# Kernel optimization log

Measured on AMD Instinct MI355X. Metric: run time of the kernel, lower is better.

The kernel has to match this reference:

```python
import jax, jax.numpy as jnp
import numpy as np

FILTERS = [1, 3, 7, 9]
BN_EPS = 1e-5


def _conv1d(x, w, b):
    # x: [B, C, L], w: [O, I, F] (torch Conv1d layout), 'same' padding for odd F
    pad = (w.shape[-1] - 1) // 2
    y = jax.lax.conv_general_dilated(
        x, w, window_strides=(1,), padding=[(pad, pad)],
        dimension_numbers=("NCH", "OIH", "NCH"))
    return y + b[None, :, None]


def _bn_elu(x, gamma, beta):
    # BatchNorm1d in training mode: biased batch stats over (batch, length)
    m = jnp.mean(x, axis=(0, 2), keepdims=True)
    v = jnp.var(x, axis=(0, 2), keepdims=True)
    xn = (x - m) * jax.lax.rsqrt(v + BN_EPS)
    return jax.nn.elu(xn * gamma[None, :, None] + beta[None, :, None])


def setup_inputs() -> dict:
    key = jax.random.key(0)
    ks = jax.random.split(key, 32)
    b, h, l, lk, dk = 8, 8, 1024, 1024, 64
    inp = {
        "Q": jax.random.normal(ks[0], (b, h, l, dk), jnp.float32),
        "K": jax.random.normal(ks[1], (b, h, lk, dk), jnp.float32),
        "V": jax.random.normal(ks[2], (b, h, lk, dk), jnp.float32),
        "W_pq": jax.random.normal(ks[3], (1, dk), jnp.float32) * 0.1,
        "W_bq": jax.random.normal(ks[4], (dk, 1), jnp.float32) * 0.1,
        "W_bk": jax.random.normal(ks[5], (dk, 1), jnp.float32) * 0.1,
        "bn_g": jax.random.uniform(ks[6], (h,), jnp.float32, 0.5, 1.5),
        "bn_b": jax.random.normal(ks[7], (h,), jnp.float32) * 0.1,
        "attn_mask": jnp.ones((1,), dtype=bool),
    }
    for i, f in enumerate(FILTERS):
        s = 1.0 / np.sqrt(h * f)
        inp[f"cq_w{i}"] = jax.random.normal(ks[8 + i], (h, h, f), jnp.float32) * s
        inp[f"cq_b{i}"] = jax.random.normal(ks[12 + i], (h,), jnp.float32) * 0.05
        inp[f"ck_w{i}"] = jax.random.normal(ks[16 + i], (h, h, f), jnp.float32) * s
        inp[f"ck_b{i}"] = jax.random.normal(ks[20 + i], (h,), jnp.float32) * 0.05
    return inp


def reference(Q, K, V, W_pq, W_bq, W_bk,
              cq_w0, cq_b0, cq_w1, cq_b1, cq_w2, cq_b2, cq_w3, cq_b3,
              ck_w0, ck_b0, ck_w1, ck_b1, ck_w2, ck_b2, ck_w3, ck_b3,
              bn_g, bn_b, attn_mask):
    b, h, l, dk = Q.shape
    lk = K.shape[2]
    nf = len(FILTERS)
    # proj_q applied to BOTH Q and K (proj_k is dead in the original code)
    q = jnp.einsum("bhld,d->bhl", Q, W_pq[0])  # [b,h,l]
    k = jnp.einsum("bhld,d->bhl", K, W_pq[0])  # [b,h,lk]
    cq = [(cq_w0, cq_b0), (cq_w1, cq_b1), (cq_w2, cq_b2), (cq_w3, cq_b3)]
    ck = [(ck_w0, ck_b0), (ck_w1, ck_b1), (ck_w2, ck_b2), (ck_w3, ck_b3)]
    Q_l = [_bn_elu(_conv1d(q, w, bb), bn_g, bn_b) for w, bb in cq]
    K_l = [_bn_elu(_conv1d(k, w, bb), bn_g, bn_b) for w, bb in ck]
    # replicate torch.cat(dim=0) + reshape(b,h,nf*len) flat-order semantics
    Q_p = jnp.concatenate(Q_l, axis=0).reshape(b, h, nf * l)    # [b,h,4l]
    K_p = jnp.concatenate(K_l, axis=0).reshape(b, h, nf * lk)   # [b,h,4lk]
    Qt = jax.lax.top_k(Q_p, l)[0]                               # [b,h,l]
    Km = jnp.mean(K_p.reshape(b, h, nf, lk), axis=2)            # [b,h,lk]
    Kt = jax.lax.top_k(Km, lk)[0]                               # descending sort
    Qb = Qt[..., None] * W_bq[:, 0]                             # [b,h,l,dk]
    Kb = Kt[..., None] * W_bk[:, 0]                             # [b,h,lk,dk]
    scores = jnp.einsum("bhqd,bhkd->bhqk", Qb, Kb) / np.float32(np.sqrt(dk))
    attn = jax.nn.softmax(scores, axis=-1)
    context = jnp.einsum("bhqk,bhkd->bhqd", attn, V)
    return context, attn
```

## Files before the change

### kernel.cpp

```cpp
#include <hip/hip_runtime.h>
#include <hip/hip_bf16.h>
#include <math.h>

namespace {
constexpr int CONV_OFF = 131072;
constexpr int PS_OFF   = 655360;
constexpr int PSS_OFF  = 659456;
constexpr int QT_OFF   = 663552;
constexpr int KT_OFF   = 729088;

typedef short bf16x8 __attribute__((ext_vector_type(8)));
typedef float f32x4 __attribute__((ext_vector_type(4)));

union BF8 {
  bf16x8 v;
  short s[8];
};

__device__ inline float bn_elu(float v, float mean, float rstd, float g,
                               float be) {
  const float x = (v - mean) * rstd * g + be;
  return x > 0.f ? x : expm1f(x);
}

__device__ inline void cswap(float& a, float& b, bool up) {
  const float mx = fmaxf(a, b), mn = fminf(a, b);
  a = up ? mx : mn;
  b = up ? mn : mx;
}

__device__ inline void wsort1024(float v[16], int lane) {
#pragma unroll
  for (int k = 2; k <= 1024; k <<= 1) {
#pragma unroll
    for (int j = 512; j >= 16; j >>= 1) {
      if (j <= (k >> 1)) {
        const int lj = j >> 4;
        const bool up = ((lane & (k >> 4)) == 0);
        const bool keep = (up == ((lane & lj) == 0));
#pragma unroll
        for (int e = 0; e < 16; ++e) {
          const float p = __shfl_xor(v[e], lj, 64);
          v[e] = keep ? fmaxf(v[e], p) : fminf(v[e], p);
        }
      }
    }
#pragma unroll
    for (int j = 8; j >= 1; j >>= 1) {
      if (j <= (k >> 1)) {
#pragma unroll
        for (int e = 0; e < 16; ++e) {
          if ((e & j) == 0) {
            bool up;
            if (k >= 32)
              up = ((lane & (k >> 4)) == 0);
            else if (k == 16)
              up = ((lane & 1) == 0);
            else
              up = ((e & k) == 0);
            cswap(v[e], v[e ^ j], up);
          }
        }
      }
    }
  }
}

__device__ inline void wmerge1024(float v[16], int lane) {
#pragma unroll
  for (int lj = 32; lj >= 1; lj >>= 1) {
    const bool keep = ((lane & lj) == 0);
#pragma unroll
    for (int e = 0; e < 16; ++e) {
      const float p = __shfl_xor(v[e], lj, 64);
      v[e] = keep ? fmaxf(v[e], p) : fminf(v[e], p);
    }
  }
#pragma unroll
  for (int j = 8; j >= 1; j >>= 1)
#pragma unroll
    for (int e = 0; e < 16; ++e)
      if ((e & j) == 0) cswap(v[e], v[e ^ j], true);
}

template <int F>
__device__ inline void pc_filter(const float* __restrict__ xs,
                                 const float* __restrict__ wsm, float bias,
                                 float* __restrict__ outp, int grp, int ln,
                                 int lq, float& sv, float& qv) {
  constexpr int pad = (F - 1) / 2;
  sv = 0.f;
  qv = 0.f;
#pragma unroll
  for (int i = 0; i < 4; ++i) {
    const int l = ln + 32 * i;
    float acc = bias;
#pragma unroll
    for (int c = 0; c < 8; ++c) {
      const float* xrow = &xs[c * 136 + l + 4 - pad];
      const float* wrow = &wsm[(grp * 8 + c) * F];
#pragma unroll
      for (int f = 0; f < F; ++f) acc = fmaf(xrow[f], wrow[f], acc);
    }
    outp[grp * 1024 + lq * 128 + l] = acc;
    sv += acc;
    qv = fmaf(acc, acc, qv);
  }
}

__global__ __launch_bounds__(256) void projconv_kernel(
    const float* __restrict__ Q, const float* __restrict__ K,
    const float* __restrict__ Wpq,
    const float* __restrict__ wq0, const float* __restrict__ bq0,
    const float* __restrict__ wq1, const float* __restrict__ bq1,
    const float* __restrict__ wq2, const float* __restrict__ bq2,
    const float* __restrict__ wq3, const float* __restrict__ bq3,
    const float* __restrict__ wk0, const float* __restrict__ bk0,
    const float* __restrict__ wk1, const float* __restrict__ bk1,
    const float* __restrict__ wk2, const float* __restrict__ bk2,
    const float* __restrict__ wk3, const float* __restrict__ bk3,
    float* __restrict__ conv, float* __restrict__ psum,
    float* __restrict__ psumsq) {
  __shared__ float xs[8 * 136];
  __shared__ float wsh[64];
  __shared__ float wsm[1280];
  __shared__ float bsm[32];
  const int tid = threadIdx.x;
  const int blk = blockIdx.x;
  const int path = blk >> 6, bb = (blk >> 3) & 7, lq = blk & 7;
  const float* X = path == 0 ? Q : K;
  const float* w0 = path == 0 ? wq0 : wk0;
  const float* w1 = path == 0 ? wq1 : wk1;
  const float* w2 = path == 0 ? wq2 : wk2;
  const float* w3 = path == 0 ? wq3 : wk3;
  const float* b0 = path == 0 ? bq0 : bk0;
  const float* b1 = path == 0 ? bq1 : bk1;
  const float* b2 = path == 0 ? bq2 : bk2;
  const float* b3 = path == 0 ? bq3 : bk3;
  if (tid < 64) wsh[tid] = Wpq[tid];
  for (int e = tid; e < 64; e += 256) wsm[e] = w0[e];
  for (int e = tid; e < 192; e += 256) wsm[64 + e] = w1[e];
  for (int e = tid; e < 448; e += 256) wsm[256 + e] = w2[e];
  for (int e = tid; e < 576; e += 256) wsm[704 + e] = w3[e];
  if (tid < 8)
    bsm[tid] = b0[tid];
  else if (tid < 16)
    bsm[tid] = b1[tid - 8];
  else if (tid < 24)
    bsm[tid] = b2[tid - 16];
  else if (tid < 32)
    bsm[tid] = b3[tid - 24];
  __syncthreads();
  for (int w = tid; w < 1088; w += 256) {
    const int c = w / 136, p = w - c * 136;
    const int gl = lq * 128 + p - 4;
    float acc = 0.f;
    if (gl >= 0 && gl < 1024) {
      const float* src = X + ((size_t)(bb * 8 + c) * 1024 + gl) * 64;
#pragma unroll
      for (int j = 0; j < 16; ++j) {
        const float4 x4 = *(const float4*)(src + j * 4);
        acc = fmaf(x4.x, wsh[j * 4 + 0], acc);
        acc = fmaf(x4.y, wsh[j * 4 + 1], acc);
        acc = fmaf(x4.z, wsh[j * 4 + 2], acc);
        acc = fmaf(x4.w, wsh[j * 4 + 3], acc);
      }
    }
    xs[c * 136 + p] = acc;
  }
  __syncthreads();
  const int grp = tid >> 5, ln = tid & 31;
  float sv, qv;
#define PC_DO(fi, F, WOFF)                                                   \
  pc_filter<F>(xs, wsm + WOFF, bsm[fi * 8 + grp],                            \
               conv + (size_t)((path * 4 + fi) * 8 + bb) * 8192, grp, ln,    \
               lq, sv, qv);                                                  \
  _Pragma("unroll") for (int m = 16; m >= 1; m >>= 1) {                      \
    sv += __shfl_xor(sv, m, 64);                                             \
    qv += __shfl_xor(qv, m, 64);                                             \
  }                                                                          \
  if (ln == 0) {                                                             \
    psum[((path * 4 + fi) * 8 + grp) * 64 + bb * 8 + lq] = sv;               \
    psumsq[((path * 4 + fi) * 8 + grp) * 64 + bb * 8 + lq] = qv;             \
  }
  PC_DO(0, 1, 0)
  PC_DO(1, 3, 64)
  PC_DO(2, 7, 256)
  PC_DO(3, 9, 704)
#undef PC_DO
}

__global__ __launch_bounds__(256) void sortmerge2_kernel(
    const float* __restrict__ conv, const float* __restrict__ psum,
    const float* __restrict__ psumsq, const float* __restrict__ bng,
    const float* __restrict__ bnb, float* __restrict__ Qt,
    float* __restrict__ Kt) {
  __shared__ float s1[1024];
  __shared__ float s2[1024];
  const int tid = threadIdx.x, blk = blockIdx.x;
  const int wv = tid >> 6, l = tid & 63;
  float v[16];
  if (blk < 64) {
    const int row = blk;
    const int hp = row & 7, fi = row >> 4;
    const int bb = ((row >> 3) & 1) * 4 + (hp >> 1);
    const int hh = (hp & 1) * 4 + wv;
    const int ch = fi * 8 + hh;
    float sval = 0.f;
    if (l < 2) {
      const float* src = (l == 0) ? psum : psumsq;
#pragma unroll
      for (int i = 0; i < 64; ++i) sval += src[ch * 64 + i];
    }
    const float mean = __shfl(sval, 0, 64) * (1.f / 8192.f);
    const float msq = __shfl(sval, 1, 64) * (1.f / 8192.f);
    const float rstd = rsqrtf(fmaxf(msq - mean * mean, 0.f) + 1e-5f);
    const float g = bng[hh], be = bnb[hh];
    const float* base = conv + (size_t)(fi * 8 + bb) * 8192 + hh * 1024;
#pragma unroll
    for (int j = 0; j < 4; ++j) {
      const float4 x = *(const float4*)&base[l * 16 + j * 4];
      v[j * 4 + 0] = bn_elu(x.x, mean, rstd, g, be);
      v[j * 4 + 1] = bn_elu(x.y, mean, rstd, g, be);
      v[j * 4 + 2] = bn_elu(x.z, mean, rstd, g, be);
      v[j * 4 + 3] = bn_elu(x.w, mean, rstd, g, be);
    }
    wsort1024(v, l);
    if (wv == 1)
#pragma unroll
      for (int e = 0; e < 16; ++e) s1[l * 16 + e] = v[e];
    if (wv == 3)
#pragma unroll
      for (int e = 0; e < 16; ++e) s2[l * 16 + e] = v[e];
    __syncthreads();
    if (wv == 0) {
#pragma unroll
      for (int e = 0; e < 16; ++e) v[e] = fmaxf(v[e], s1[1023 - (l * 16 + e)]);
      wmerge1024(v, l);
    } else if (wv == 2) {
#pragma unroll
      for (int e = 0; e < 16; ++e) v[e] = fmaxf(v[e], s2[1023 - (l * 16 + e)]);
      wmerge1024(v, l);
#pragma unroll
      for (int e = 0; e < 16; ++e) s2[l * 16 + e] = v[e];
    }
    __syncthreads();
    if (wv == 0) {
#pragma unroll
      for (int e = 0; e < 16; ++e) v[e] = fmaxf(v[e], s2[1023 - (l * 16 + e)]);
      wmerge1024(v, l);
      float* qd = Qt + (size_t)row * 1024 + l * 16;
#pragma unroll
      for (int j = 0; j < 4; ++j)
        *(float4*)&qd[j * 4] =
            make_float4(v[j * 4], v[j * 4 + 1], v[j * 4 + 2], v[j * 4 + 3]);
    }
  } else {
    const int row = (blk - 64) * 4 + wv;
    const int hp = row & 7, fi = row >> 4;
    const int bb = ((row >> 3) & 1) * 4 + (hp >> 1);
    const int chk = 32 + fi * 8 + (hp & 1) * 4;
    float sval = 0.f;
    if (l < 8) {
      const float* src = (l < 4) ? psum : psumsq;
      const int ch = chk + (l & 3);
#pragma unroll
      for (int i = 0; i < 64; ++i) sval += src[ch * 64 + i];
    }
    float cm[4], cr[4];
#pragma unroll
    for (int j = 0; j < 4; ++j) {
      const float mean = __shfl(sval, j, 64) * (1.f / 8192.f);
      const float msq = __shfl(sval, j + 4, 64) * (1.f / 8192.f);
      cm[j] = mean;
      cr[j] = rsqrtf(fmaxf(msq - mean * mean, 0.f) + 1e-5f);
    }
#pragma unroll
    for (int e = 0; e < 16; ++e) v[e] = 0.f;
#pragma unroll
    for (int j = 0; j < 4; ++j) {
      const int hh = (hp & 1) * 4 + j;
      const float g = bng[hh], be = bnb[hh];
      const float* base =
          conv + (size_t)(4 + fi) * 64 * 1024 + (size_t)bb * 8192 + hh * 1024;
#pragma unroll
      for (int jj = 0; jj < 4; ++jj) {
        const float4 x = *(const float4*)&base[l * 16 + jj * 4];
        v[jj * 4 + 0] += bn_elu(x.x, cm[j], cr[j], g, be);
        v[jj * 4 + 1] += bn_elu(x.y, cm[j], cr[j], g, be);
        v[jj * 4 + 2] += bn_elu(x.z, cm[j], cr[j], g, be);
        v[jj * 4 + 3] += bn_elu(x.w, cm[j], cr[j], g, be);
      }
    }
#pragma unroll
    for (int e = 0; e < 16; ++e) v[e] *= 0.25f;
    wsort1024(v, l);
    float* kd = Kt + (size_t)row * 1024 + l * 16;
#pragma unroll
    for (int j = 0; j < 4; ++j)
      *(float4*)&kd[j * 4] =
          make_float4(v[j * 4], v[j * 4 + 1], v[j * 4 + 2], v[j * 4 + 3]);
  }
}

__global__ __launch_bounds__(256, 4) void attn5_kernel(
    const float* __restrict__ V, const float* __restrict__ Qt,
    const float* __restrict__ Kt, const float* __restrict__ Wbq,
    const float* __restrict__ Wbk, float* __restrict__ ctx,
    float* __restrict__ attn) {
  __shared__ float Kts[1024];
  __shared__ float sq[64], mq[64], rz[64];
  __shared__ short Vhi[2][8 * 64 * 8];
  __shared__ short Vlo[2][8 * 64 * 8];
  const int tid = threadIdx.x;
  const int b = blockIdx.x;
  const int bh = ((b & 7) << 3) | ((b >> 3) & 7);
  const int qt = b >> 6;
  const int qbase = qt * 64;
  const int lane0 = tid & 63;
  float cval;
  {
    float d = Wbq[lane0] * Wbk[lane0];
#pragma unroll
    for (int mm = 32; mm >= 1; mm >>= 1) d += __shfl_xor(d, mm, 64);
    cval = d * 0.125f;
  }
  const float* Ktg = Kt + (size_t)bh * 1024;
  for (int t = tid; t < 1024; t += 256) Kts[t] = Ktg[t];
  const float kHi = Ktg[0], kLo = Ktg[1023];
  if (tid < 64) {
    const float s = cval * Qt[(size_t)bh * 1024 + qbase + tid];
    sq[tid] = s;
    mq[tid] = fmaxf(s * kHi, s * kLo);
  }
  __syncthreads();
  {
    const int row = tid >> 2, qtr = tid & 3;
    const float s = sq[row], m = mq[row];
    float z = 0.f;
    const int k0 = qtr * 256;
    for (int k = 0; k < 256; ++k) z += __expf(fmaf(s, Kts[k0 + k], -m));
    z += __shfl_xor(z, 1, 64);
    z += __shfl_xor(z, 2, 64);
    if (qtr == 0) rz[row] = 1.f / z;
  }
  __syncthreads();

  const int wv = tid >> 6, l = tid & 63;
  const int l15 = l & 15, l4 = l >> 4;
  const int q = wv * 16 + l15;
  const float s = sq[q], m = mq[q], r = rz[q];
  f32x4 acc[4];
#pragma unroll
  for (int dt = 0; dt < 4; ++dt) acc[dt] = (f32x4){0.f, 0.f, 0.f, 0.f};

  const float* Vb = V + (size_t)bh * 65536;
  float* arow = attn + ((size_t)bh << 20) + (size_t)qbase * 1024;
  const int dV = tid & 63, kqV = tid >> 6;

  for (int ch = 0; ch < 16; ++ch) {
    const int kc = ch * 64;
    const int buf = ch & 1;
    float vreg[2][8];
#pragma unroll
    for (int g = 0; g < 2; ++g) {
      const int ko = kqV + g * 4;
      const float* vs = Vb + (size_t)(kc + ko * 8) * 64 + dV;
#pragma unroll
      for (int i = 0; i < 8; ++i) vreg[g][i] = vs[i * 64];
    }
    bf16x8 ahi[2], alo[2];
#pragma unroll
    for (int ks = 0; ks < 2; ++ks) {
      const int kb = kc + ks * 32 + l4 * 8;
      const float4 kv0 = *(const float4*)&Kts[kb];
      const float4 kv1 = *(const float4*)&Kts[kb + 4];
      float e[8];
      e[0] = __expf(fmaf(s, kv0.x, -m)) * r;
      e[1] = __expf(fmaf(s, kv0.y, -m)) * r;
      e[2] = __expf(fmaf(s, kv0.z, -m)) * r;
      e[3] = __expf(fmaf(s, kv0.w, -m)) * r;
      e[4] = __expf(fmaf(s, kv1.x, -m)) * r;
      e[5] = __expf(fmaf(s, kv1.y, -m)) * r;
      e[6] = __expf(fmaf(s, kv1.z, -m)) * r;
      e[7] = __expf(fmaf(s, kv1.w, -m)) * r;
      float* ag = arow + (size_t)q * 1024 + kb;
      *(float4*)ag = make_float4(e[0], e[1], e[2], e[3]);
      *(float4*)(ag + 4) = make_float4(e[4], e[5], e[6], e[7]);
      BF8 H, L;
#pragma unroll
      for (int i = 0; i < 8; ++i) {
        const __hip_bfloat16 hb = __float2bfloat16(e[i]);
        H.s[i] = __bfloat16_as_short(hb);
        L.s[i] =
            __bfloat16_as_short(__float2bfloat16(e[i] - __bfloat162float(hb)));
      }
      ahi[ks] = H.v;
      alo[ks] = L.v;
    }
#pragma unroll
    for (int g = 0; g < 2; ++g) {
      const int ko = kqV + g * 4;
      BF8 H, L;
#pragma unroll
      for (int i = 0; i < 8; ++i) {
        const float f = vreg[g][i];
        const __hip_bfloat16 hb = __float2bfloat16(f);
        H.s[i] = __bfloat16_as_short(hb);
        L.s[i] =
            __bfloat16_as_short(__float2bfloat16(f - __bfloat162float(hb)));
      }
      *(bf16x8*)&Vhi[buf][(ko * 64 + dV) * 8] = H.v;
      *(bf16x8*)&Vlo[buf][(ko * 64 + dV) * 8] = L.v;
    }
    __syncthreads();
#pragma unroll
    for (int ks = 0; ks < 2; ++ks) {
      const int ko = ks * 4 + l4;
#pragma unroll
      for (int dt = 0; dt < 4; ++dt) {
        const bf16x8 bhv =
            *(const bf16x8*)&Vhi[buf][(ko * 64 + dt * 16 + l15) * 8];
        const bf16x8 blv =
            *(const bf16x8*)&Vlo[buf][(ko * 64 + dt * 16 + l15) * 8];
        acc[dt] = __builtin_amdgcn_mfma_f32_16x16x32_bf16(ahi[ks], bhv,
                                                          acc[dt], 0, 0, 0);
        acc[dt] = __builtin_amdgcn_mfma_f32_16x16x32_bf16(ahi[ks], blv,
                                                          acc[dt], 0, 0, 0);
        acc[dt] = __builtin_amdgcn_mfma_f32_16x16x32_bf16(alo[ks], bhv,
                                                          acc[dt], 0, 0, 0);
      }
    }
  }
  float* cb = ctx + ((size_t)bh * 1024 + qbase + wv * 16 + l4 * 4) * 64 + l15;
#pragma unroll
  for (int dt = 0; dt < 4; ++dt)
#pragma unroll
    for (int rr = 0; rr < 4; ++rr) cb[(size_t)rr * 64 + dt * 16] = acc[dt][rr];
}

}

extern "C" void kernel_launch(void* const* d_in, const int* in_sizes, int n_in,
                              void* d_out, int out_size, void* d_ws,
                              size_t ws_size, hipStream_t stream) {
  const float* Q = (const float*)d_in[0];
  const float* K = (const float*)d_in[1];
  const float* V = (const float*)d_in[2];
  const float* Wpq = (const float*)d_in[3];
  const float* Wbq = (const float*)d_in[4];
  const float* Wbk = (const float*)d_in[5];
  const float* bng = (const float*)d_in[6];
  const float* bnb = (const float*)d_in[7];
  const float* cqw[4] = {(const float*)d_in[9], (const float*)d_in[13],
                         (const float*)d_in[17], (const float*)d_in[21]};
  const float* cqb[4] = {(const float*)d_in[10], (const float*)d_in[14],
                         (const float*)d_in[18], (const float*)d_in[22]};
  const float* ckw[4] = {(const float*)d_in[11], (const float*)d_in[15],
                         (const float*)d_in[19], (const float*)d_in[23]};
  const float* ckb[4] = {(const float*)d_in[12], (const float*)d_in[16],
                         (const float*)d_in[20], (const float*)d_in[24]};

  float* ws = (float*)d_ws;
  float* conv = ws + CONV_OFF;
  float* psum = ws + PS_OFF;
  float* psumsq = ws + PSS_OFF;
  float* Qtp = ws + QT_OFF;
  float* Ktp = ws + KT_OFF;
  float* ctx = (float*)d_out;
  float* attn = ctx + (size_t)8 * 8 * 1024 * 64;

  projconv_kernel<<<128, 256, 0, stream>>>(
      Q, K, Wpq, cqw[0], cqb[0], cqw[1], cqb[1], cqw[2], cqb[2], cqw[3],
      cqb[3], ckw[0], ckb[0], ckw[1], ckb[1], ckw[2], ckb[2], ckw[3], ckb[3],
      conv, psum, psumsq);
  sortmerge2_kernel<<<80, 256, 0, stream>>>(conv, psum, psumsq, bng, bnb, Qtp,
                                            Ktp);
  attn5_kernel<<<1024, 256, 0, stream>>>(V, Qtp, Ktp, Wbq, Wbk, ctx, attn);
}
```

Measured before the change: 116.8 us.

## Split projection-conv into finer tiles and spread K-path averaging across waves

Halves the sequence tile per projconv block (64 instead of 128 positions), doubling the grid to 256 blocks, and doubles the partial-sum slots to match. In the sort kernel, the K path now gives each row its own block, with four waves each doing the BN+ELU for one channel in parallel and combining through shared memory before one wave sorts. It also compacts the workspace offsets. The aim is more parallelism in the two pre-attention stages, at the cost of more halo recomputation, more partial sums to reduce, and an extra barrier.

New measurement: 110.2 us. 1.06x faster.

```diff
diff --git a/kernel.cpp b/kernel.cpp
--- a/kernel.cpp
+++ b/kernel.cpp
@@ -3,11 +3,11 @@
 #include <math.h>
 
 namespace {
-constexpr int CONV_OFF = 131072;
-constexpr int PS_OFF   = 655360;
-constexpr int PSS_OFF  = 659456;
-constexpr int QT_OFF   = 663552;
-constexpr int KT_OFF   = 729088;
+constexpr int CONV_OFF = 0;
+constexpr int PS_OFF   = 524288;
+constexpr int PSS_OFF  = 532480;
+constexpr int QT_OFF   = 540672;
+constexpr int KT_OFF   = 606208;
 
 typedef short bf16x8 __attribute__((ext_vector_type(8)));
 typedef float f32x4 __attribute__((ext_vector_type(4)));
@@ -92,17 +92,17 @@
   sv = 0.f;
   qv = 0.f;
 #pragma unroll
-  for (int i = 0; i < 4; ++i) {
+  for (int i = 0; i < 2; ++i) {
     const int l = ln + 32 * i;
     float acc = bias;
 #pragma unroll
     for (int c = 0; c < 8; ++c) {
-      const float* xrow = &xs[c * 136 + l + 4 - pad];
+      const float* xrow = &xs[c * 72 + l + 4 - pad];
       const float* wrow = &wsm[(grp * 8 + c) * F];
 #pragma unroll
       for (int f = 0; f < F; ++f) acc = fmaf(xrow[f], wrow[f], acc);
     }
-    outp[grp * 1024 + lq * 128 + l] = acc;
+    outp[grp * 1024 + lq * 64 + l] = acc;
     sv += acc;
     qv = fmaf(acc, acc, qv);
   }
@@ -121,13 +121,13 @@
     const float* __restrict__ wk3, const float* __restrict__ bk3,
     float* __restrict__ conv, float* __restrict__ psum,
     float* __restrict__ psumsq) {
-  __shared__ float xs[8 * 136];
+  __shared__ float xs[8 * 72];
   __shared__ float wsh[64];
   __shared__ float wsm[1280];
   __shared__ float bsm[32];
   const int tid = threadIdx.x;
   const int blk = blockIdx.x;
-  const int path = blk >> 6, bb = (blk >> 3) & 7, lq = blk & 7;
+  const int path = blk >> 7, bb = (blk >> 4) & 7, lq = blk & 15;
   const float* X = path == 0 ? Q : K;
   const float* w0 = path == 0 ? wq0 : wk0;
   const float* w1 = path == 0 ? wq1 : wk1;
@@ -151,9 +151,9 @@
   else if (tid < 32)
     bsm[tid] = b3[tid - 24];
   __syncthreads();
-  for (int w = tid; w < 1088; w += 256) {
-    const int c = w / 136, p = w - c * 136;
-    const int gl = lq * 128 + p - 4;
+  for (int w = tid; w < 576; w += 256) {
+    const int c = w / 72, p = w - c * 72;
+    const int gl = lq * 64 + p - 4;
     float acc = 0.f;
     if (gl >= 0 && gl < 1024) {
       const float* src = X + ((size_t)(bb * 8 + c) * 1024 + gl) * 64;
@@ -166,7 +166,7 @@
         acc = fmaf(x4.w, wsh[j * 4 + 3], acc);
       }
     }
-    xs[c * 136 + p] = acc;
+    xs[c * 72 + p] = acc;
   }
   __syncthreads();
   const int grp = tid >> 5, ln = tid & 31;
@@ -180,8 +180,8 @@
     qv += __shfl_xor(qv, m, 64);                                             \
   }                                                                          \
   if (ln == 0) {                                                             \
-    psum[((path * 4 + fi) * 8 + grp) * 64 + bb * 8 + lq] = sv;               \
-    psumsq[((path * 4 + fi) * 8 + grp) * 64 + bb * 8 + lq] = qv;             \
+    psum[((path * 4 + fi) * 8 + grp) * 128 + bb * 16 + lq] = sv;             \
+    psumsq[((path * 4 + fi) * 8 + grp) * 128 + bb * 16 + lq] = qv;           \
   }
   PC_DO(0, 1, 0)
   PC_DO(1, 3, 64)
@@ -190,13 +190,15 @@
 #undef PC_DO
 }
 
-__global__ __launch_bounds__(256) void sortmerge2_kernel(
+__global__ __launch_bounds__(256) void sortmerge3_kernel(
     const float* __restrict__ conv, const float* __restrict__ psum,
     const float* __restrict__ psumsq, const float* __restrict__ bng,
     const float* __restrict__ bnb, float* __restrict__ Qt,
     float* __restrict__ Kt) {
   __shared__ float s1[1024];
   __shared__ float s2[1024];
+  __shared__ float s3[1024];
+  __shared__ float s4[1024];
   const int tid = threadIdx.x, blk = blockIdx.x;
   const int wv = tid >> 6, l = tid & 63;
   float v[16];
@@ -210,7 +212,7 @@
     if (l < 2) {
       const float* src = (l == 0) ? psum : psumsq;
 #pragma unroll
-      for (int i = 0; i < 64; ++i) sval += src[ch * 64 + i];
+      for (int i = 0; i < 128; ++i) sval += src[ch * 128 + i];
     }
     const float mean = __shfl(sval, 0, 64) * (1.f / 8192.f);
     const float msq = __shfl(sval, 1, 64) * (1.f / 8192.f);
@@ -256,50 +258,49 @@
             make_float4(v[j * 4], v[j * 4 + 1], v[j * 4 + 2], v[j * 4 + 3]);
     }
   } else {
-    const int row = (blk - 64) * 4 + wv;
+    const int row = blk - 64;
     const int hp = row & 7, fi = row >> 4;
     const int bb = ((row >> 3) & 1) * 4 + (hp >> 1);
-    const int chk = 32 + fi * 8 + (hp & 1) * 4;
+    const int hh = (hp & 1) * 4 + wv;
+    const int ch = 32 + fi * 8 + hh;
     float sval = 0.f;
-    if (l < 8) {
-      const float* src = (l < 4) ? psum : psumsq;
-      const int ch = chk + (l & 3);
-#pragma unroll
-      for (int i = 0; i < 64; ++i) sval += src[ch * 64 + i];
-    }
-    float cm[4], cr[4];
+    if (l < 2) {
+      const float* src = (l == 0) ? psum : psumsq;
+#pragma unroll
+      for (int i = 0; i < 128; ++i) sval += src[ch * 128 + i];
+    }
+    const float mean = __shfl(sval, 0, 64) * (1.f / 8192.f);
+    const float msq = __shfl(sval, 1, 64) * (1.f / 8192.f);
+    const float rstd = rsqrtf(fmaxf(msq - mean * mean, 0.f) + 1e-5f);
+    const float g = bng[hh], be = bnb[hh];
+    const float* base =
+        conv + (size_t)(4 + fi) * 65536 + (size_t)bb * 8192 + hh * 1024;
+    float t16[16];
 #pragma unroll
     for (int j = 0; j < 4; ++j) {
-      const float mean = __shfl(sval, j, 64) * (1.f / 8192.f);
-      const float msq = __shfl(sval, j + 4, 64) * (1.f / 8192.f);
-      cm[j] = mean;
-      cr[j] = rsqrtf(fmaxf(msq - mean * mean, 0.f) + 1e-5f);
-    }
-#pragma unroll
-    for (int e = 0; e < 16; ++e) v[e] = 0.f;
-#pragma unroll
-    for (int j = 0; j < 4; ++j) {
-      const int hh = (hp & 1) * 4 + j;
-      const float g = bng[hh], be = bnb[hh];
-      const float* base =
-          conv + (size_t)(4 + fi) * 64 * 1024 + (size_t)bb * 8192 + hh * 1024;
-#pragma unroll
-      for (int jj = 0; jj < 4; ++jj) {
-        const float4 x = *(const float4*)&base[l * 16 + jj * 4];
-        v[jj * 4 + 0] += bn_elu(x.x, cm[j], cr[j], g, be);
-        v[jj * 4 + 1] += bn_elu(x.y, cm[j], cr[j], g, be);
-        v[jj * 4 + 2] += bn_elu(x.z, cm[j], cr[j], g, be);
-        v[jj * 4 + 3] += bn_elu(x.w, cm[j], cr[j], g, be);
-      }
-    }
-#pragma unroll
-    for (int e = 0; e < 16; ++e) v[e] *= 0.25f;
-    wsort1024(v, l);
-    float* kd = Kt + (size_t)row * 1024 + l * 16;
-#pragma unroll
-    for (int j = 0; j < 4; ++j)
-      *(float4*)&kd[j * 4] =
-          make_float4(v[j * 4], v[j * 4 + 1], v[j * 4 + 2], v[j * 4 + 3]);
+      const float4 x = *(const float4*)&base[l * 16 + j * 4];
+      t16[j * 4 + 0] = bn_elu(x.x, mean, rstd, g, be);
+      t16[j * 4 + 1] = bn_elu(x.y, mean, rstd, g, be);
+      t16[j * 4 + 2] = bn_elu(x.z, mean, rstd, g, be);
+      t16[j * 4 + 3] = bn_elu(x.w, mean, rstd, g, be);
+    }
+    float* dst = wv == 0 ? s1 : wv == 1 ? s2 : wv == 2 ? s3 : s4;
+#pragma unroll
+    for (int e = 0; e < 16; ++e) dst[l * 16 + e] = t16[e];
+    __syncthreads();
+    if (wv == 0) {
+#pragma unroll
+      for (int e = 0; e < 16; ++e)
+        v[e] = ((s1[l * 16 + e] + s2[l * 16 + e]) + s3[l * 16 + e] +
+                s4[l * 16 + e]) *
+               0.25f;
+      wsort1024(v, l);
+      float* kd = Kt + (size_t)row * 1024 + l * 16;
+#pragma unroll
+      for (int j = 0; j < 4; ++j)
+        *(float4*)&kd[j * 4] =
+            make_float4(v[j * 4], v[j * 4 + 1], v[j * 4 + 2], v[j * 4 + 3]);
+    }
   }
 }
 
@@ -470,11 +471,11 @@
   float* ctx = (float*)d_out;
   float* attn = ctx + (size_t)8 * 8 * 1024 * 64;
 
-  projconv_kernel<<<128, 256, 0, stream>>>(
+  projconv_kernel<<<256, 256, 0, stream>>>(
       Q, K, Wpq, cqw[0], cqb[0], cqw[1], cqb[1], cqw[2], cqb[2], cqw[3],
       cqb[3], ckw[0], ckb[0], ckw[1], ckb[1], ckw[2], ckb[2], ckw[3], ckb[3],
       conv, psum, psumsq);
-  sortmerge2_kernel<<<80, 256, 0, stream>>>(conv, psum, psumsq, bng, bnb, Qtp,
-                                            Ktp);
+  sortmerge3_kernel<<<128, 256, 0, stream>>>(conv, psum, psumsq, bng, bnb,
+                                             Qtp, Ktp);
   attn5_kernel<<<1024, 256, 0, stream>>>(V, Qtp, Ktp, Wbq, Wbk, ctx, attn);
 }
```
